# Performance work log

Measured on AMD Instinct MI355X. Metric: run time of the kernel, lower is better.

## Reference

```python
import jax, jax.numpy as jnp
import numpy as np

D = 256
N_EDGES = 8192
N_CORNERS = 4096


def setup_inputs() -> dict:
    key = jax.random.key(0)
    ks = jax.random.split(key, 8)
    scale = 1.0 / np.sqrt(D)
    return {
        "edge_pred": jax.random.uniform(ks[0], (N_EDGES,), dtype=jnp.float32),
        "edge_corner": jax.random.randint(ks[1], (N_EDGES, 2), 0, N_CORNERS, dtype=jnp.int64),
        "all_corners": jax.random.uniform(ks[2], (N_CORNERS, 2), dtype=jnp.float32),
        "edge_x": jax.random.normal(ks[3], (N_EDGES, D), dtype=jnp.float32),
        "image_x": jax.random.normal(ks[4], (1024,), dtype=jnp.float32),
        "W1": jax.random.normal(ks[5], (D, D), dtype=jnp.float32) * scale,
        "b1": jnp.zeros((D,), dtype=jnp.float32),
        "W2": jax.random.normal(ks[6], (D, D), dtype=jnp.float32) * scale,
        "b2": jnp.zeros((D,), dtype=jnp.float32),
        "W3": jax.random.normal(ks[7], (3 * D, D), dtype=jnp.float32) * scale,
        "b3": jnp.zeros((D,), dtype=jnp.float32),
    }


def _linear_block(x, W, b):
    # LinearBlock: Linear followed by ReLU
    return jax.nn.relu(x @ W + b)


def reference(edge_pred, edge_corner, all_corners, edge_x, image_x, W1, b1, W2, b2, W3, b3):
    # 'fully' branch of MPModule.forward. edge_pred/edge_corner/all_corners/image_x
    # are unused in this branch (kept for signature fidelity).
    e1 = _linear_block(edge_x, W1, b1)              # [N, D]
    # (e1.unsqueeze(1) * e1).mean(-1) == (e1 @ e1.T) / D   -> [N, N]
    sim1 = (e1 @ e1.T) / D
    e2 = _linear_block(edge_x, W2, b2)
    sim2 = (e2 @ e2.T) / D
    # (edge_x * sim.unsqueeze(-1)).sum(1) == sim @ edge_x  -> [N, D]
    agg1 = sim1 @ edge_x
    agg2 = sim2 @ edge_x
    cat = jnp.concatenate([edge_x, agg1, agg2], axis=-1)  # [N, 3D]
    out = _linear_block(cat, W3, b3)                      # [N, D]
    return out
```

## Files before the change

kernel.cpp:

```cpp
#include <hip/hip_runtime.h>

#define NE 8192
#define DD 256
#define NSPLIT 32

typedef __attribute__((ext_vector_type(8))) short short8;
typedef __attribute__((ext_vector_type(4))) short short4v;
typedef __attribute__((ext_vector_type(8))) __bf16 bf16x8;
typedef __attribute__((ext_vector_type(4))) float floatx4;

__device__ __forceinline__ unsigned short f2bf(float f) {
  union { float f; unsigned int i; } v; v.f = f;
  unsigned int r = v.i + 0x7fffu + ((v.i >> 16) & 1u);
  return (unsigned short)(r >> 16);
}

__device__ __forceinline__ floatx4 mfma_bf16(short8 a, short8 b, floatx4 c) {
  return __builtin_amdgcn_mfma_f32_16x16x32_bf16(
      __builtin_bit_cast(bf16x8, a), __builtin_bit_cast(bf16x8, b), c, 0, 0, 0);
}

__global__ __launch_bounds__(256, 3)
void e_gemm(const float* __restrict__ x,
            const float* __restrict__ W1, const float* __restrict__ b1,
            const float* __restrict__ W2, const float* __restrict__ b2,
            unsigned short* __restrict__ e1, unsigned short* __restrict__ e2,
            unsigned short* __restrict__ e1T, unsigned short* __restrict__ e2T,
            unsigned short* __restrict__ xT)
{
  __shared__ __align__(16) unsigned short smA[64 * 136];
  __shared__ __align__(16) unsigned short smB1[64 * 136];
  __shared__ __align__(16) unsigned short smB2[64 * 136];
  const int T = threadIdx.x, lane = T & 63, wv = T >> 6;
  const int q = lane >> 4, r = lane & 15;
  const int col0 = blockIdx.x * 64, row0 = blockIdx.y * 64;
  const bool emit = ((int)blockIdx.x == (int)(blockIdx.y & 3));

  floatx4 acc1[4], acc2[4];
#pragma unroll
  for (int j = 0; j < 4; ++j) {
    acc1[j] = (floatx4){0.f, 0.f, 0.f, 0.f};
    acc2[j] = (floatx4){0.f, 0.f, 0.f, 0.f};
  }

  for (int kc = 0; kc < 256; kc += 128) {
#pragma unroll
    for (int p = 0; p < 8; ++p) {
      const int id = p * 256 + T, rr = id >> 5, k4 = (id & 31) * 4;
      floatx4 v = *(const floatx4*)&x[(size_t)(row0 + rr) * DD + kc + k4];
      short4v s;
#pragma unroll
      for (int c = 0; c < 4; ++c) s[c] = (short)f2bf(v[c]);
      *(short4v*)&smA[rr * 136 + k4] = s;
    }
#pragma unroll
    for (int p = 0; p < 2; ++p) {
      const int id = p * 256 + T, kb = id >> 4, n4 = id & 15;
      floatx4 w1r[4], w2r[4];
#pragma unroll
      for (int i = 0; i < 4; ++i) {
        w1r[i] = *(const floatx4*)&W1[(size_t)(kc + kb * 4 + i) * DD + col0 + n4 * 4];
        w2r[i] = *(const floatx4*)&W2[(size_t)(kc + kb * 4 + i) * DD + col0 + n4 * 4];
      }
#pragma unroll
      for (int s4 = 0; s4 < 4; ++s4) {
        const int c = (s4 + n4) & 3;
        short4v s1 = {(short)f2bf(w1r[0][c]), (short)f2bf(w1r[1][c]),
                      (short)f2bf(w1r[2][c]), (short)f2bf(w1r[3][c])};
        short4v s2 = {(short)f2bf(w2r[0][c]), (short)f2bf(w2r[1][c]),
                      (short)f2bf(w2r[2][c]), (short)f2bf(w2r[3][c])};
        *(short4v*)&smB1[(n4 * 4 + c) * 136 + kb * 4] = s1;
        *(short4v*)&smB2[(n4 * 4 + c) * 136 + kb * 4] = s2;
      }
    }
    __syncthreads();
#pragma unroll
    for (int ks = 0; ks < 4; ++ks) {
      short8 af = *(const short8*)&smA[(wv * 16 + r) * 136 + ks * 32 + q * 8];
#pragma unroll
      for (int j = 0; j < 4; ++j) {
        short8 b1f = *(const short8*)&smB1[(j * 16 + r) * 136 + ks * 32 + q * 8];
        short8 b2f = *(const short8*)&smB2[(j * 16 + r) * 136 + ks * 32 + q * 8];
        acc1[j] = mfma_bf16(af, b1f, acc1[j]);
        acc2[j] = mfma_bf16(af, b2f, acc2[j]);
      }
    }
    if (emit) {
#pragma unroll
      for (int p = 0; p < 4; ++p) {
        const int id = p * 256 + T, kk = id >> 3, r8 = (id & 7) * 8;
        short8 v;
#pragma unroll
        for (int i = 0; i < 8; ++i) v[i] = (short)smA[(r8 + i) * 136 + kk];
        *(short8*)&xT[(size_t)(kc + kk) * NE + row0 + r8] = v;
      }
    }
    __syncthreads();
  }

#pragma unroll
  for (int j = 0; j < 4; ++j) {
    const int col = col0 + j * 16 + r;
    const int rowb = row0 + wv * 16 + q * 4;
    const float b1v = b1[col], b2v = b2[col];
    short4v t1, t2;
#pragma unroll
    for (int t = 0; t < 4; ++t) {
      unsigned short h1 = f2bf(fmaxf(acc1[j][t] + b1v, 0.0f));
      unsigned short h2 = f2bf(fmaxf(acc2[j][t] + b2v, 0.0f));
      t1[t] = (short)h1; t2[t] = (short)h2;
      e1[(size_t)(rowb + t) * DD + col] = h1;
      e2[(size_t)(rowb + t) * DD + col] = h2;
    }
    *(short4v*)&e1T[(size_t)col * NE + rowb] = t1;
    *(short4v*)&e2T[(size_t)col * NE + rowb] = t2;
  }
}

__global__ __launch_bounds__(256, 4)
void atb(const unsigned short* __restrict__ e1T, const unsigned short* __restrict__ e2T,
         const unsigned short* __restrict__ xT, float* __restrict__ P_T)
{
  __shared__ __align__(16) unsigned short smA[64 * 136];
  __shared__ __align__(16) unsigned short smB[64 * 136];
  const int T = threadIdx.x, lane = T & 63, wv = T >> 6;
  const int q = lane >> 4, r = lane & 15;
  const int m0 = (blockIdx.x >> 2) * 64, n0 = (blockIdx.x & 3) * 64;
  const int y = blockIdx.y, z = blockIdx.z;
  const int j0 = y * (NE / NSPLIT);
  const unsigned short* E = z ? e2T : e1T;
  float* P = P_T + (size_t)(z * NSPLIT + y) * 65536;

  floatx4 acc[4];
#pragma unroll
  for (int j = 0; j < 4; ++j) acc[j] = (floatx4){0.f, 0.f, 0.f, 0.f};

  for (int jc = 0; jc < NE / NSPLIT; jc += 128) {
#pragma unroll
    for (int p = 0; p < 4; ++p) {
      const int id = p * 256 + T, mm = id >> 4, j8 = (id & 15) * 8;
      *(short8*)&smA[mm * 136 + j8] =
          *(const short8*)&E[(size_t)(m0 + mm) * NE + j0 + jc + j8];
      *(short8*)&smB[mm * 136 + j8] =
          *(const short8*)&xT[(size_t)(n0 + mm) * NE + j0 + jc + j8];
    }
    __syncthreads();
#pragma unroll
    for (int ks = 0; ks < 4; ++ks) {
      short8 af = *(const short8*)&smA[(wv * 16 + r) * 136 + ks * 32 + q * 8];
#pragma unroll
      for (int j = 0; j < 4; ++j) {
        short8 bf = *(const short8*)&smB[(j * 16 + r) * 136 + ks * 32 + q * 8];
        acc[j] = mfma_bf16(af, bf, acc[j]);
      }
    }
    __syncthreads();
  }
#pragma unroll
  for (int j = 0; j < 4; ++j) {
    const int n = n0 + j * 16 + r;
    const int m = m0 + wv * 16 + q * 4;
    *(floatx4*)&P[(size_t)n * DD + m] = acc[j];
  }
}

__global__ void reduce_g(const float* __restrict__ P_T, float* __restrict__ G_T) {
  int idx = blockIdx.x * 256 + threadIdx.x;
  int z = idx >> 14, off = idx & 16383;
  const floatx4* Pp = (const floatx4*)P_T;
  floatx4 s = (floatx4){0.f, 0.f, 0.f, 0.f};
#pragma unroll
  for (int y = 0; y < NSPLIT; ++y)
    s += Pp[(size_t)(z * NSPLIT + y) * 16384 + off];
  ((floatx4*)G_T)[idx] = s;
}

__global__ __launch_bounds__(256, 2)
void h_mfma(const float* __restrict__ G_T, const float* __restrict__ W3,
            unsigned short* __restrict__ H1t, unsigned short* __restrict__ H2t)
{
  __shared__ __align__(16) unsigned short smA[64 * 136];
  __shared__ __align__(16) unsigned short smB[64 * 136];
  const int T = threadIdx.x, lane = T & 63, wv = T >> 6;
  const int q = lane >> 4, r = lane & 15;
  const int z = blockIdx.z;
  const int me0 = (blockIdx.x >> 2) * 64, m30 = (blockIdx.x & 3) * 64;
  const float* G = G_T + (size_t)z * 65536;
  unsigned short* Ht = z ? H2t : H1t;
  const int woff = 256 + z * 256;

  floatx4 acc[4];
#pragma unroll
  for (int j = 0; j < 4; ++j) acc[j] = (floatx4){0.f, 0.f, 0.f, 0.f};

  for (int lc = 0; lc < 256; lc += 128) {
#pragma unroll
    for (int p = 0; p < 2; ++p) {
      const int id = p * 256 + T, lb = id >> 4, e4 = id & 15;
      floatx4 grow[4], wrow[4];
#pragma unroll
      for (int i = 0; i < 4; ++i) {
        grow[i] = *(const floatx4*)&G[(size_t)(lc + lb * 4 + i) * DD + me0 + e4 * 4];
        wrow[i] = *(const floatx4*)&W3[(size_t)(woff + lc + lb * 4 + i) * DD + m30 + e4 * 4];
      }
#pragma unroll
      for (int s4 = 0; s4 < 4; ++s4) {
        const int c = (s4 + e4) & 3;
        short4v ga = {(short)f2bf(grow[0][c] * 0.00390625f),
                      (short)f2bf(grow[1][c] * 0.00390625f),
                      (short)f2bf(grow[2][c] * 0.00390625f),
                      (short)f2bf(grow[3][c] * 0.00390625f)};
        short4v wa = {(short)f2bf(wrow[0][c]), (short)f2bf(wrow[1][c]),
                      (short)f2bf(wrow[2][c]), (short)f2bf(wrow[3][c])};
        *(short4v*)&smA[(e4 * 4 + c) * 136 + lb * 4] = ga;
        *(short4v*)&smB[(e4 * 4 + c) * 136 + lb * 4] = wa;
      }
    }
    __syncthreads();
#pragma unroll
    for (int ks = 0; ks < 4; ++ks) {
      short8 af = *(const short8*)&smA[(wv * 16 + r) * 136 + ks * 32 + q * 8];
#pragma unroll
      for (int j = 0; j < 4; ++j) {
        short8 bf = *(const short8*)&smB[(j * 16 + r) * 136 + ks * 32 + q * 8];
        acc[j] = mfma_bf16(af, bf, acc[j]);
      }
    }
    __syncthreads();
  }
#pragma unroll
  for (int j = 0; j < 4; ++j) {
    const int m3 = m30 + j * 16 + r;
    const int me = me0 + wv * 16 + q * 4;
    short4v v;
#pragma unroll
    for (int i = 0; i < 4; ++i) v[i] = (short)f2bf(acc[j][i]);
    *(short4v*)&Ht[(size_t)m3 * DD + me] = v;
  }
}

__global__ __launch_bounds__(256, 4)
void out_gemm(const float* __restrict__ x,
              const unsigned short* __restrict__ e1, const unsigned short* __restrict__ e2,
              const float* __restrict__ W3,
              const unsigned short* __restrict__ H1t, const unsigned short* __restrict__ H2t,
              const float* __restrict__ b3, float* __restrict__ out)
{
  __shared__ __align__(16) unsigned short smA[64 * 136];
  __shared__ __align__(16) unsigned short smB[64 * 136];
  const int T = threadIdx.x, lane = T & 63, wv = T >> 6;
  const int q = lane >> 4, r = lane & 15;
  const int col0 = blockIdx.x * 64, row0 = blockIdx.y * 64;

  floatx4 acc[4];
#pragma unroll
  for (int j = 0; j < 4; ++j) acc[j] = (floatx4){0.f, 0.f, 0.f, 0.f};

  for (int s = 0; s < 3; ++s) {
    for (int kc = 0; kc < 256; kc += 128) {
      if (s == 0) {
#pragma unroll
        for (int p = 0; p < 8; ++p) {
          const int id = p * 256 + T, rr = id >> 5, k4 = (id & 31) * 4;
          floatx4 v = *(const floatx4*)&x[(size_t)(row0 + rr) * DD + kc + k4];
          short4v sv;
#pragma unroll
          for (int c = 0; c < 4; ++c) sv[c] = (short)f2bf(v[c]);
          *(short4v*)&smA[rr * 136 + k4] = sv;
        }
#pragma unroll
        for (int p = 0; p < 2; ++p) {
          const int id = p * 256 + T, kb = id >> 4, n4 = id & 15;
          floatx4 wrow[4];
#pragma unroll
          for (int i = 0; i < 4; ++i)
            wrow[i] = *(const floatx4*)&W3[(size_t)(kc + kb * 4 + i) * DD + col0 + n4 * 4];
#pragma unroll
          for (int s4 = 0; s4 < 4; ++s4) {
            const int c = (s4 + n4) & 3;
            short4v sv = {(short)f2bf(wrow[0][c]), (short)f2bf(wrow[1][c]),
                          (short)f2bf(wrow[2][c]), (short)f2bf(wrow[3][c])};
            *(short4v*)&smB[(n4 * 4 + c) * 136 + kb * 4] = sv;
          }
        }
      } else {
        const unsigned short* E = (s == 1) ? e1 : e2;
        const unsigned short* Hs = (s == 1) ? H1t : H2t;
#pragma unroll
        for (int p = 0; p < 4; ++p) {
          const int id = p * 256 + T, rr = id >> 4, j8 = (id & 15) * 8;
          *(short8*)&smA[rr * 136 + j8] =
              *(const short8*)&E[(size_t)(row0 + rr) * DD + kc + j8];
          *(short8*)&smB[rr * 136 + j8] =
              *(const short8*)&Hs[(size_t)(col0 + rr) * DD + kc + j8];
        }
      }
      __syncthreads();
#pragma unroll
      for (int ks = 0; ks < 4; ++ks) {
        short8 af = *(const short8*)&smA[(wv * 16 + r) * 136 + ks * 32 + q * 8];
#pragma unroll
        for (int j = 0; j < 4; ++j) {
          short8 bf = *(const short8*)&smB[(j * 16 + r) * 136 + ks * 32 + q * 8];
          acc[j] = mfma_bf16(af, bf, acc[j]);
        }
      }
      __syncthreads();
    }
  }
#pragma unroll
  for (int j = 0; j < 4; ++j) {
    const int col = col0 + j * 16 + r;
    const float bv = b3[col];
    const int rowb = row0 + wv * 16 + q * 4;
#pragma unroll
    for (int t = 0; t < 4; ++t)
      out[(size_t)(rowb + t) * DD + col] = fmaxf(acc[j][t] + bv, 0.0f);
  }
}

extern "C" void kernel_launch(void* const* d_in, const int* in_sizes, int n_in,
                              void* d_out, int out_size, void* d_ws, size_t ws_size,
                              hipStream_t stream) {
  (void)in_sizes; (void)n_in; (void)out_size; (void)ws_size;
  const float* x  = (const float*)d_in[3];
  const float* W1 = (const float*)d_in[5];
  const float* b1 = (const float*)d_in[6];
  const float* W2 = (const float*)d_in[7];
  const float* b2 = (const float*)d_in[8];
  const float* W3 = (const float*)d_in[9];
  const float* b3 = (const float*)d_in[10];
  float* out = (float*)d_out;

  char* ws = (char*)d_ws;
  const size_t MB = 1u << 20;
  const size_t KB = 1u << 10;
  unsigned short* e1  = (unsigned short*)ws;
  unsigned short* e2  = (unsigned short*)(ws + 4 * MB);
  unsigned short* e1T = (unsigned short*)(ws + 8 * MB);
  unsigned short* e2T = (unsigned short*)(ws + 12 * MB);
  unsigned short* xT  = (unsigned short*)(ws + 16 * MB);
  unsigned short* H1t = (unsigned short*)(ws + 20 * MB);
  unsigned short* H2t = (unsigned short*)(ws + 20 * MB + 128 * KB);
  float* G_T          = (float*)(ws + 20 * MB + 256 * KB);
  float* P_T          = (float*)(ws + 21 * MB);

  e_gemm<<<dim3(4, 128), 256, 0, stream>>>(x, W1, b1, W2, b2, e1, e2, e1T, e2T, xT);
  atb<<<dim3(16, NSPLIT, 2), 256, 0, stream>>>(e1T, e2T, xT, P_T);
  reduce_g<<<128, 256, 0, stream>>>(P_T, G_T);
  h_mfma<<<dim3(16, 1, 2), 256, 0, stream>>>(G_T, W3, H1t, H2t);
  out_gemm<<<dim3(4, 128), 256, 0, stream>>>(x, e1, e2, W3, H1t, H2t, b3, out);
}
```

Measured before the change: 134.7 us.

## Pre-convert inputs to bf16 in one pass and enlarge atb M tile

```diff
diff --git a/kernel.cpp b/kernel.cpp
--- a/kernel.cpp
+++ b/kernel.cpp
@@ -20,13 +20,65 @@
       __builtin_bit_cast(bf16x8, a), __builtin_bit_cast(bf16x8, b), c, 0, 0, 0);
 }
 
+__device__ __forceinline__ void tcvt_tile(const float* __restrict__ src, int C,
+                                          unsigned short* __restrict__ dst, int R,
+                                          int r0, int c0, int tid) {
+  __shared__ float ls[64][68];
+  const int rr = tid >> 4;
+  const int c4 = (tid & 15) * 4;
+#pragma unroll
+  for (int k = 0; k < 4; ++k)
+    *(floatx4*)&ls[rr + k * 16][c4] =
+        *(const floatx4*)&src[(size_t)(r0 + rr + k * 16) * C + c0 + c4];
+  __syncthreads();
+  const int cc = tid >> 2;
+  const int rb = (tid & 3) * 16;
+  short8 o0, o1;
+#pragma unroll
+  for (int i = 0; i < 8; ++i) {
+    o0[i] = (short)f2bf(ls[rb + i][cc]);
+    o1[i] = (short)f2bf(ls[rb + 8 + i][cc]);
+  }
+  unsigned short* dp = &dst[(size_t)(c0 + cc) * R + r0 + rb];
+  *(short8*)dp = o0;
+  *(short8*)(dp + 8) = o1;
+}
+
+__global__ void cvt_all(const float* __restrict__ x, unsigned short* __restrict__ xb,
+                        unsigned short* __restrict__ xT,
+                        const float* __restrict__ W1, unsigned short* __restrict__ W1t,
+                        const float* __restrict__ W2, unsigned short* __restrict__ W2t,
+                        const float* __restrict__ W3, unsigned short* __restrict__ W3t0) {
+  const int b = blockIdx.x, tid = threadIdx.x;
+  if (b < 1024) {
+    int i = b * 256 + tid;
+    floatx4 a = ((const floatx4*)x)[2 * i];
+    floatx4 c = ((const floatx4*)x)[2 * i + 1];
+    short8 o;
+#pragma unroll
+    for (int k = 0; k < 4; ++k) { o[k] = (short)f2bf(a[k]); o[4 + k] = (short)f2bf(c[k]); }
+    ((short8*)xb)[i] = o;
+  } else if (b < 1536) {
+    int t = b - 1024;
+    tcvt_tile(x, DD, xT, NE, (t >> 2) * 64, (t & 3) * 64, tid);
+  } else if (b < 1552) {
+    int t = b - 1536;
+    tcvt_tile(W1, DD, W1t, DD, (t >> 2) * 64, (t & 3) * 64, tid);
+  } else if (b < 1568) {
+    int t = b - 1552;
+    tcvt_tile(W2, DD, W2t, DD, (t >> 2) * 64, (t & 3) * 64, tid);
+  } else {
+    int t = b - 1568;
+    tcvt_tile(W3, DD, W3t0, DD, (t >> 2) * 64, (t & 3) * 64, tid);
+  }
+}
+
 __global__ __launch_bounds__(256, 3)
-void e_gemm(const float* __restrict__ x,
-            const float* __restrict__ W1, const float* __restrict__ b1,
-            const float* __restrict__ W2, const float* __restrict__ b2,
+void e_gemm(const unsigned short* __restrict__ xb,
+            const unsigned short* __restrict__ W1t, const float* __restrict__ b1,
+            const unsigned short* __restrict__ W2t, const float* __restrict__ b2,
             unsigned short* __restrict__ e1, unsigned short* __restrict__ e2,
-            unsigned short* __restrict__ e1T, unsigned short* __restrict__ e2T,
-            unsigned short* __restrict__ xT)
+            unsigned short* __restrict__ e1T, unsigned short* __restrict__ e2T)
 {
   __shared__ __align__(16) unsigned short smA[64 * 136];
   __shared__ __align__(16) unsigned short smB1[64 * 136];
@@ -34,7 +86,6 @@
   const int T = threadIdx.x, lane = T & 63, wv = T >> 6;
   const int q = lane >> 4, r = lane & 15;
   const int col0 = blockIdx.x * 64, row0 = blockIdx.y * 64;
-  const bool emit = ((int)blockIdx.x == (int)(blockIdx.y & 3));
 
   floatx4 acc1[4], acc2[4];
 #pragma unroll
@@ -45,33 +96,14 @@
 
   for (int kc = 0; kc < 256; kc += 128) {
 #pragma unroll
-    for (int p = 0; p < 8; ++p) {
-      const int id = p * 256 + T, rr = id >> 5, k4 = (id & 31) * 4;
-      floatx4 v = *(const floatx4*)&x[(size_t)(row0 + rr) * DD + kc + k4];
-      short4v s;
-#pragma unroll
-      for (int c = 0; c < 4; ++c) s[c] = (short)f2bf(v[c]);
-      *(short4v*)&smA[rr * 136 + k4] = s;
-    }
-#pragma unroll
-    for (int p = 0; p < 2; ++p) {
-      const int id = p * 256 + T, kb = id >> 4, n4 = id & 15;
-      floatx4 w1r[4], w2r[4];
-#pragma unroll
-      for (int i = 0; i < 4; ++i) {
-        w1r[i] = *(const floatx4*)&W1[(size_t)(kc + kb * 4 + i) * DD + col0 + n4 * 4];
-        w2r[i] = *(const floatx4*)&W2[(size_t)(kc + kb * 4 + i) * DD + col0 + n4 * 4];
-      }
-#pragma unroll
-      for (int s4 = 0; s4 < 4; ++s4) {
-        const int c = (s4 + n4) & 3;
-        short4v s1 = {(short)f2bf(w1r[0][c]), (short)f2bf(w1r[1][c]),
-                      (short)f2bf(w1r[2][c]), (short)f2bf(w1r[3][c])};
-        short4v s2 = {(short)f2bf(w2r[0][c]), (short)f2bf(w2r[1][c]),
-                      (short)f2bf(w2r[2][c]), (short)f2bf(w2r[3][c])};
-        *(short4v*)&smB1[(n4 * 4 + c) * 136 + kb * 4] = s1;
-        *(short4v*)&smB2[(n4 * 4 + c) * 136 + kb * 4] = s2;
-      }
+    for (int p = 0; p < 4; ++p) {
+      const int id = p * 256 + T, rr = id >> 4, k8 = (id & 15) * 8;
+      *(short8*)&smA[rr * 136 + k8] =
+          *(const short8*)&xb[(size_t)(row0 + rr) * DD + kc + k8];
+      *(short8*)&smB1[rr * 136 + k8] =
+          *(const short8*)&W1t[(size_t)(col0 + rr) * DD + kc + k8];
+      *(short8*)&smB2[rr * 136 + k8] =
+          *(const short8*)&W2t[(size_t)(col0 + rr) * DD + kc + k8];
     }
     __syncthreads();
 #pragma unroll
@@ -83,16 +115,6 @@
         short8 b2f = *(const short8*)&smB2[(j * 16 + r) * 136 + ks * 32 + q * 8];
         acc1[j] = mfma_bf16(af, b1f, acc1[j]);
         acc2[j] = mfma_bf16(af, b2f, acc2[j]);
-      }
-    }
-    if (emit) {
-#pragma unroll
-      for (int p = 0; p < 4; ++p) {
-        const int id = p * 256 + T, kk = id >> 3, r8 = (id & 7) * 8;
-        short8 v;
-#pragma unroll
-        for (int i = 0; i < 8; ++i) v[i] = (short)smA[(r8 + i) * 136 + kk];
-        *(short8*)&xT[(size_t)(kc + kk) * NE + row0 + r8] = v;
       }
     }
     __syncthreads();
@@ -117,51 +139,65 @@
   }
 }
 
-__global__ __launch_bounds__(256, 4)
+__global__ __launch_bounds__(256, 3)
 void atb(const unsigned short* __restrict__ e1T, const unsigned short* __restrict__ e2T,
          const unsigned short* __restrict__ xT, float* __restrict__ P_T)
 {
-  __shared__ __align__(16) unsigned short smA[64 * 136];
+  __shared__ __align__(16) unsigned short smA[128 * 136];
   __shared__ __align__(16) unsigned short smB[64 * 136];
   const int T = threadIdx.x, lane = T & 63, wv = T >> 6;
   const int q = lane >> 4, r = lane & 15;
-  const int m0 = (blockIdx.x >> 2) * 64, n0 = (blockIdx.x & 3) * 64;
+  const int m0 = (blockIdx.x >> 2) * 128, n0 = (blockIdx.x & 3) * 64;
   const int y = blockIdx.y, z = blockIdx.z;
   const int j0 = y * (NE / NSPLIT);
   const unsigned short* E = z ? e2T : e1T;
   float* P = P_T + (size_t)(z * NSPLIT + y) * 65536;
 
-  floatx4 acc[4];
-#pragma unroll
-  for (int j = 0; j < 4; ++j) acc[j] = (floatx4){0.f, 0.f, 0.f, 0.f};
+  floatx4 acc[2][4];
+#pragma unroll
+  for (int i = 0; i < 2; ++i)
+#pragma unroll
+    for (int j = 0; j < 4; ++j) acc[i][j] = (floatx4){0.f, 0.f, 0.f, 0.f};
 
   for (int jc = 0; jc < NE / NSPLIT; jc += 128) {
 #pragma unroll
-    for (int p = 0; p < 4; ++p) {
+    for (int p = 0; p < 8; ++p) {
       const int id = p * 256 + T, mm = id >> 4, j8 = (id & 15) * 8;
       *(short8*)&smA[mm * 136 + j8] =
           *(const short8*)&E[(size_t)(m0 + mm) * NE + j0 + jc + j8];
-      *(short8*)&smB[mm * 136 + j8] =
-          *(const short8*)&xT[(size_t)(n0 + mm) * NE + j0 + jc + j8];
+    }
+#pragma unroll
+    for (int p = 0; p < 4; ++p) {
+      const int id = p * 256 + T, nn = id >> 4, j8 = (id & 15) * 8;
+      *(short8*)&smB[nn * 136 + j8] =
+          *(const short8*)&xT[(size_t)(n0 + nn) * NE + j0 + jc + j8];
     }
     __syncthreads();
 #pragma unroll
     for (int ks = 0; ks < 4; ++ks) {
-      short8 af = *(const short8*)&smA[(wv * 16 + r) * 136 + ks * 32 + q * 8];
-#pragma unroll
-      for (int j = 0; j < 4; ++j) {
-        short8 bf = *(const short8*)&smB[(j * 16 + r) * 136 + ks * 32 + q * 8];
-        acc[j] = mfma_bf16(af, bf, acc[j]);
-      }
-    }
-    __syncthreads();
-  }
-#pragma unroll
-  for (int j = 0; j < 4; ++j) {
-    const int n = n0 + j * 16 + r;
-    const int m = m0 + wv * 16 + q * 4;
-    *(floatx4*)&P[(size_t)n * DD + m] = acc[j];
-  }
+      short8 af[2], bf[4];
+#pragma unroll
+      for (int i = 0; i < 2; ++i)
+        af[i] = *(const short8*)&smA[(wv * 32 + i * 16 + r) * 136 + ks * 32 + q * 8];
+#pragma unroll
+      for (int j = 0; j < 4; ++j)
+        bf[j] = *(const short8*)&smB[(j * 16 + r) * 136 + ks * 32 + q * 8];
+#pragma unroll
+      for (int i = 0; i < 2; ++i)
+#pragma unroll
+        for (int j = 0; j < 4; ++j)
+          acc[i][j] = mfma_bf16(af[i], bf[j], acc[i][j]);
+    }
+    __syncthreads();
+  }
+#pragma unroll
+  for (int i = 0; i < 2; ++i)
+#pragma unroll
+    for (int j = 0; j < 4; ++j) {
+      const int n = n0 + j * 16 + r;
+      const int m = m0 + wv * 32 + i * 16 + q * 4;
+      *(floatx4*)&P[(size_t)n * DD + m] = acc[i][j];
+    }
 }
 
 __global__ void reduce_g(const float* __restrict__ P_T, float* __restrict__ G_T) {
@@ -239,10 +275,10 @@
   }
 }
 
-__global__ __launch_bounds__(256, 4)
-void out_gemm(const float* __restrict__ x,
+__global__ __launch_bounds__(256, 3)
+void out_gemm(const unsigned short* __restrict__ xb,
               const unsigned short* __restrict__ e1, const unsigned short* __restrict__ e2,
-              const float* __restrict__ W3,
+              const unsigned short* __restrict__ W3t0,
               const unsigned short* __restrict__ H1t, const unsigned short* __restrict__ H2t,
               const float* __restrict__ b3, float* __restrict__ out)
 {
@@ -256,57 +292,32 @@
 #pragma unroll
   for (int j = 0; j < 4; ++j) acc[j] = (floatx4){0.f, 0.f, 0.f, 0.f};
 
-  for (int s = 0; s < 3; ++s) {
-    for (int kc = 0; kc < 256; kc += 128) {
-      if (s == 0) {
-#pragma unroll
-        for (int p = 0; p < 8; ++p) {
-          const int id = p * 256 + T, rr = id >> 5, k4 = (id & 31) * 4;
-          floatx4 v = *(const floatx4*)&x[(size_t)(row0 + rr) * DD + kc + k4];
-          short4v sv;
-#pragma unroll
-          for (int c = 0; c < 4; ++c) sv[c] = (short)f2bf(v[c]);
-          *(short4v*)&smA[rr * 136 + k4] = sv;
-        }
-#pragma unroll
-        for (int p = 0; p < 2; ++p) {
-          const int id = p * 256 + T, kb = id >> 4, n4 = id & 15;
-          floatx4 wrow[4];
-#pragma unroll
-          for (int i = 0; i < 4; ++i)
-            wrow[i] = *(const floatx4*)&W3[(size_t)(kc + kb * 4 + i) * DD + col0 + n4 * 4];
-#pragma unroll
-          for (int s4 = 0; s4 < 4; ++s4) {
-            const int c = (s4 + n4) & 3;
-            short4v sv = {(short)f2bf(wrow[0][c]), (short)f2bf(wrow[1][c]),
-                          (short)f2bf(wrow[2][c]), (short)f2bf(wrow[3][c])};
-            *(short4v*)&smB[(n4 * 4 + c) * 136 + kb * 4] = sv;
-          }
-        }
-      } else {
-        const unsigned short* E = (s == 1) ? e1 : e2;
-        const unsigned short* Hs = (s == 1) ? H1t : H2t;
-#pragma unroll
-        for (int p = 0; p < 4; ++p) {
-          const int id = p * 256 + T, rr = id >> 4, j8 = (id & 15) * 8;
-          *(short8*)&smA[rr * 136 + j8] =
-              *(const short8*)&E[(size_t)(row0 + rr) * DD + kc + j8];
-          *(short8*)&smB[rr * 136 + j8] =
-              *(const short8*)&Hs[(size_t)(col0 + rr) * DD + kc + j8];
-        }
-      }
-      __syncthreads();
-#pragma unroll
-      for (int ks = 0; ks < 4; ++ks) {
-        short8 af = *(const short8*)&smA[(wv * 16 + r) * 136 + ks * 32 + q * 8];
-#pragma unroll
-        for (int j = 0; j < 4; ++j) {
-          short8 bf = *(const short8*)&smB[(j * 16 + r) * 136 + ks * 32 + q * 8];
-          acc[j] = mfma_bf16(af, bf, acc[j]);
-        }
-      }
-      __syncthreads();
-    }
+  const unsigned short* As[3] = {xb, e1, e2};
+  const unsigned short* Bs[3] = {W3t0, H1t, H2t};
+
+  for (int rd = 0; rd < 6; ++rd) {
+    const int s = rd >> 1, kc = (rd & 1) * 128;
+    const unsigned short* A = As[s];
+    const unsigned short* B = Bs[s];
+#pragma unroll
+    for (int p = 0; p < 4; ++p) {
+      const int id = p * 256 + T, rr = id >> 4, k8 = (id & 15) * 8;
+      *(short8*)&smA[rr * 136 + k8] =
+          *(const short8*)&A[(size_t)(row0 + rr) * DD + kc + k8];
+      *(short8*)&smB[rr * 136 + k8] =
+          *(const short8*)&B[(size_t)(col0 + rr) * DD + kc + k8];
+    }
+    __syncthreads();
+#pragma unroll
+    for (int ks = 0; ks < 4; ++ks) {
+      short8 af = *(const short8*)&smA[(wv * 16 + r) * 136 + ks * 32 + q * 8];
+#pragma unroll
+      for (int j = 0; j < 4; ++j) {
+        short8 bf = *(const short8*)&smB[(j * 16 + r) * 136 + ks * 32 + q * 8];
+        acc[j] = mfma_bf16(af, bf, acc[j]);
+      }
+    }
+    __syncthreads();
   }
 #pragma unroll
   for (int j = 0; j < 4; ++j) {
@@ -335,19 +346,24 @@
   char* ws = (char*)d_ws;
   const size_t MB = 1u << 20;
   const size_t KB = 1u << 10;
-  unsigned short* e1  = (unsigned short*)ws;
-  unsigned short* e2  = (unsigned short*)(ws + 4 * MB);
-  unsigned short* e1T = (unsigned short*)(ws + 8 * MB);
-  unsigned short* e2T = (unsigned short*)(ws + 12 * MB);
-  unsigned short* xT  = (unsigned short*)(ws + 16 * MB);
-  unsigned short* H1t = (unsigned short*)(ws + 20 * MB);
-  unsigned short* H2t = (unsigned short*)(ws + 20 * MB + 128 * KB);
-  float* G_T          = (float*)(ws + 20 * MB + 256 * KB);
-  float* P_T          = (float*)(ws + 21 * MB);
-
-  e_gemm<<<dim3(4, 128), 256, 0, stream>>>(x, W1, b1, W2, b2, e1, e2, e1T, e2T, xT);
-  atb<<<dim3(16, NSPLIT, 2), 256, 0, stream>>>(e1T, e2T, xT, P_T);
+  unsigned short* xb   = (unsigned short*)ws;
+  unsigned short* xT   = (unsigned short*)(ws + 4 * MB);
+  unsigned short* e1   = (unsigned short*)(ws + 8 * MB);
+  unsigned short* e2   = (unsigned short*)(ws + 12 * MB);
+  unsigned short* e1T  = (unsigned short*)(ws + 16 * MB);
+  unsigned short* e2T  = (unsigned short*)(ws + 20 * MB);
+  unsigned short* W1t  = (unsigned short*)(ws + 24 * MB);
+  unsigned short* W2t  = (unsigned short*)(ws + 24 * MB + 128 * KB);
+  unsigned short* W3t0 = (unsigned short*)(ws + 24 * MB + 256 * KB);
+  unsigned short* H1t  = (unsigned short*)(ws + 24 * MB + 384 * KB);
+  unsigned short* H2t  = (unsigned short*)(ws + 24 * MB + 512 * KB);
+  float* G_T           = (float*)(ws + 24 * MB + 640 * KB);
+  float* P_T           = (float*)(ws + 25 * MB);
+
+  cvt_all<<<1584, 256, 0, stream>>>(x, xb, xT, W1, W1t, W2, W2t, W3, W3t0);
+  e_gemm<<<dim3(4, 128), 256, 0, stream>>>(xb, W1t, b1, W2t, b2, e1, e2, e1T, e2T);
+  atb<<<dim3(8, NSPLIT, 2), 256, 0, stream>>>(e1T, e2T, xT, P_T);
   reduce_g<<<128, 256, 0, stream>>>(P_T, G_T);
   h_mfma<<<dim3(16, 1, 2), 256, 0, stream>>>(G_T, W3, H1t, H2t);
-  out_gemm<<<dim3(4, 128), 256, 0, stream>>>(x, e1, e2, W3, H1t, H2t, b3, out);
-}
+  out_gemm<<<dim3(4, 128), 256, 0, stream>>>(xb, e1, e2, W3t0, H1t, H2t, b3, out);
+}
```

New measurement: 126.0 us. 6.5% less time.
